# Kernel optimization log

Hardware: AMD Instinct MI355X
Metric: run time of the kernel (lower is better)

Reference implementation:

```python
import jax, jax.numpy as jnp
import numpy as np

BASE_BITS = 17            # tokens < 2**17; pack n-gram tuple into one int64
NGRAM_SIZES = (2, 3)      # sorted(ngram_to_size.keys())
TABLE_SIZE = 100000       # ngram_to_size[n]
ID_OFFSET = 4             # vocab ids start at 4 in the original
B, S, VOCAB = 256, 16384, 50000


def _encode_windows(x, n):
    """x: [B,S] int tokens -> [B,S] int64, each entry encodes the left-padded
    n-gram window (t[i-n+1],...,t[i]) exactly like the original tuple key."""
    b, s = x.shape
    padded = jnp.pad(x.astype(jnp.int64), ((0, 0), (n - 1, 0)))  # constant 0 pad, as in np.pad
    enc = jnp.zeros((b, s), dtype=jnp.int64)
    for i in range(n):  # tiny fixed loop over window size
        enc = (enc << BASE_BITS) | padded[:, i:i + s]
    return enc


def _lookup(enc, keys, vals):
    """dict.get(tuple(window), 0) as sorted-array hash-probe: searchsorted + verify."""
    flat = enc.reshape(-1)
    idx = jnp.clip(jnp.searchsorted(keys, flat), 0, keys.shape[0] - 1)
    hit = keys[idx] == flat
    return jnp.where(hit, vals[idx], 0).reshape(enc.shape)


def setup_inputs() -> dict:
    rng = np.random.default_rng(0)
    x = rng.integers(0, VOCAB, size=(B, S), dtype=np.int64)
    inp = {"x": jnp.asarray(x)}
    xj = jnp.asarray(x)
    for n in NGRAM_SIZES:
        # Build vocab tables from n-grams actually present so lookups hit,
        # mirroring update_from_batch() having seen similar data.
        enc = np.asarray(_encode_windows(xj, n)).reshape(-1)
        uniq = np.unique(enc)
        take = min(TABLE_SIZE, uniq.size)
        keys = np.sort(rng.choice(uniq, size=take, replace=False)).astype(np.int64)
        vals = (rng.permutation(take) + ID_OFFSET).astype(np.int64)  # ids 4..take+3
        inp[f"keys{n}"] = jnp.asarray(keys)
        inp[f"vals{n}"] = jnp.asarray(vals)
    return inp


def reference(x, keys2, vals2, keys3, vals3):
    tables = {2: (keys2, vals2), 3: (keys3, vals3)}
    # encode_token_ngrams + stack_ngrams -> [len(NGRAM_SIZES), B, S]
    outs = [_lookup(_encode_windows(x, n), *tables[n]) for n in NGRAM_SIZES]
    return jnp.stack(outs, axis=0)
```

## Files before the change

kernel.cpp:

```cpp
#include <hip/hip_runtime.h>

#define BASE_BITS 17
#define BUCKET_LOG 16
#define NBUCKETS (1u << BUCKET_LOG)
#define NSLOTS (NBUCKETS * 4u)
#define SLOT_MASK (NSLOTS - 1u)
#define BUCKET_MASK (NBUCKETS - 1u)
#define EMPTY 0xFFFFFFFFu

typedef int  iv4 __attribute__((ext_vector_type(4)));
typedef unsigned uv4 __attribute__((ext_vector_type(4)));

__device__ __forceinline__ unsigned bucket_of(unsigned k) {
    return (k * 2654435761u) >> (32 - BUCKET_LOG);
}

__device__ __forceinline__ int match4(uv4 q, unsigned e, unsigned b) {
    int slot = -1;
    slot = (q.w == e) ? (int)(b * 4u + 3u) : slot;
    slot = (q.z == e) ? (int)(b * 4u + 2u) : slot;
    slot = (q.y == e) ? (int)(b * 4u + 1u) : slot;
    slot = (q.x == e) ? (int)(b * 4u + 0u) : slot;
    if (slot >= 0) return slot;
    unsigned mx = max(max(q.x, q.y), max(q.z, q.w));
    return (mx == EMPTY) ? -2 : -1;
}

__global__ void clear_tables_kernel(uv4* __restrict__ dst, unsigned n4) {
    unsigned i = blockIdx.x * blockDim.x + threadIdx.x;
    unsigned stride = gridDim.x * blockDim.x;
    uv4 ones = { EMPTY, EMPTY, EMPTY, EMPTY };
    for (; i < n4; i += stride) __builtin_nontemporal_store(ones, &dst[i]);
}

__global__ void detect_dtype_kernel(const unsigned* __restrict__ xw,
                                    int* __restrict__ flags) {
    __shared__ int nz;
    if (threadIdx.x == 0) nz = 0;
    __syncthreads();
    if (xw[2 * threadIdx.x + 1] != 0u) atomicOr(&nz, 1);
    __syncthreads();
    if (threadIdx.x == 0) { flags[0] = nz ? 0 : ~0; flags[1] = 0; }
}

__global__ void build_hash_kernel(const int* __restrict__ keys2,
                                  const int* __restrict__ vals2, int n2,
                                  const int* __restrict__ keys3,
                                  const int* __restrict__ vals3, int n3,
                                  const unsigned* __restrict__ xw,
                                  unsigned* __restrict__ K2, int* __restrict__ V2,
                                  unsigned* __restrict__ K3, int* __restrict__ V3,
                                  int* __restrict__ flags) {
    int i = blockIdx.x * blockDim.x + threadIdx.x;
    if (i < 256 && xw[2 * i + 1] != 0u) atomicAnd(&flags[0], 0);

    const int* keys; const int* vals; unsigned* K; int* V; int idx;
    if (i < n2)           { keys = keys2; vals = vals2; K = K2; V = V2; idx = i; }
    else if (i < n2 + n3) { keys = keys3; vals = vals3; K = K3; V = V3; idx = i - n2; }
    else return;
    unsigned k = (unsigned)keys[idx];
    if (k == EMPTY) { atomicAnd(&flags[1], 0); return; }
    unsigned slot = bucket_of(k) * 4u;
    for (;;) {
        unsigned prev = atomicCAS(&K[slot], EMPTY, k);
        if (prev == EMPTY) { V[slot] = vals[idx]; break; }
        slot = (slot + 1u) & SLOT_MASK;
    }
}

template <typename K>
__device__ __forceinline__ int lower_bound(const K* __restrict__ keys, int n, K key) {
    int lo = 0, hi = n;
    while (lo < hi) {
        int mid = (lo + hi) >> 1;
        if (keys[mid] < key) lo = mid + 1; else hi = mid;
    }
    return lo;
}

template <typename K>
__device__ __forceinline__ K bprobe(const K* __restrict__ keys,
                                    const K* __restrict__ vals, int n, K key) {
    int idx = lower_bound(keys, n, key);
    if (idx >= n) idx = n - 1;
    return (keys[idx] == key) ? vals[idx] : (K)0;
}

__global__ __launch_bounds__(256) void ngram_hash_kernel(
    const void* __restrict__ xv,
    const unsigned* __restrict__ K2, const int* __restrict__ V2,
    const unsigned* __restrict__ K3, const int* __restrict__ V3,
    const void* __restrict__ k2v, const void* __restrict__ v2v,
    const void* __restrict__ k3v, const void* __restrict__ v3v,
    void* __restrict__ outv,
    int n2, int n3, int S, int total, const int* __restrict__ flags)
{
    int gid = blockIdx.x * blockDim.x + threadIdx.x;
    int base = gid * 4;
    if (base >= total) return;
    int f0 = flags[0], f1 = flags[1];

    if (f0 != 0) {
        const long long* x = (const long long*)xv;
        long long* out = (long long*)outv;
        for (int i = 0; i < 4 && base + i < total; ++i) {
            int g = base + i;
            int s = g & (S - 1);
            long long t2 = x[g];
            long long t1 = (s >= 1) ? x[g - 1] : 0ll;
            long long t0 = (s >= 2) ? x[g - 2] : 0ll;
            long long e2 = (t1 << BASE_BITS) | t2;
            long long e3 = (((t0 << BASE_BITS) | t1) << BASE_BITS) | t2;
            out[g]         = bprobe((const long long*)k2v, (const long long*)v2v, n2, e2);
            out[total + g] = bprobe((const long long*)k3v, (const long long*)v3v, n3, e3);
        }
        return;
    }
    if (f1 == 0) {
        const int* x = (const int*)xv;
        int* out = (int*)outv;
        for (int i = 0; i < 4 && base + i < total; ++i) {
            int g = base + i;
            int s = g & (S - 1);
            unsigned t2 = (unsigned)x[g];
            unsigned t1 = (s >= 1) ? (unsigned)x[g - 1] : 0u;
            unsigned t0 = (s >= 2) ? (unsigned)x[g - 2] : 0u;
            int e2 = (int)((t1 << BASE_BITS) | t2);
            int e3 = (int)((((t0 << BASE_BITS) | t1) << BASE_BITS) | t2);
            out[g]         = bprobe((const int*)k2v, (const int*)v2v, n2, e2);
            out[total + g] = bprobe((const int*)k3v, (const int*)v3v, n3, e3);
        }
        return;
    }

    const int* x = (const int*)xv;
    iv4 xq = __builtin_nontemporal_load(&((const iv4*)x)[gid]);
    int sb = base & (S - 1);
    unsigned t[6];
    t[0] = (sb != 0) ? (unsigned)x[base - 2] : 0u;
    t[1] = (sb != 0) ? (unsigned)x[base - 1] : 0u;
    t[2] = (unsigned)xq.x; t[3] = (unsigned)xq.y;
    t[4] = (unsigned)xq.z; t[5] = (unsigned)xq.w;

    unsigned e[8], b[8];
    #pragma unroll
    for (int i = 0; i < 4; ++i) {
        unsigned t0 = t[i], t1 = t[i + 1], t2 = t[i + 2];
        e[i]     = (t1 << BASE_BITS) | t2;
        e[i + 4] = (((t0 << BASE_BITS) | t1) << BASE_BITS) | t2;
    }
    #pragma unroll
    for (int i = 0; i < 8; ++i) b[i] = bucket_of(e[i]);

    const uv4* KB2 = (const uv4*)K2;
    const uv4* KB3 = (const uv4*)K3;

    const uv4* a0 = KB2 + b[0]; const uv4* a1 = KB2 + b[1];
    const uv4* a2 = KB2 + b[2]; const uv4* a3 = KB2 + b[3];
    const uv4* a4 = KB3 + b[4]; const uv4* a5 = KB3 + b[5];
    const uv4* a6 = KB3 + b[6]; const uv4* a7 = KB3 + b[7];
    uv4 q0, q1, q2, q3, q4, q5, q6, q7;
    asm volatile(
        "global_load_dwordx4 %0, %8, off\n\t"
        "global_load_dwordx4 %1, %9, off\n\t"
        "global_load_dwordx4 %2, %10, off\n\t"
        "global_load_dwordx4 %3, %11, off\n\t"
        "global_load_dwordx4 %4, %12, off\n\t"
        "global_load_dwordx4 %5, %13, off\n\t"
        "global_load_dwordx4 %6, %14, off\n\t"
        "global_load_dwordx4 %7, %15, off\n\t"
        "s_waitcnt vmcnt(0)"
        : "=&v"(q0), "=&v"(q1), "=&v"(q2), "=&v"(q3),
          "=&v"(q4), "=&v"(q5), "=&v"(q6), "=&v"(q7)
        : "v"(a0), "v"(a1), "v"(a2), "v"(a3),
          "v"(a4), "v"(a5), "v"(a6), "v"(a7)
        : "memory");

    int st[8];
    st[0] = match4(q0, e[0], b[0]);
    st[1] = match4(q1, e[1], b[1]);
    st[2] = match4(q2, e[2], b[2]);
    st[3] = match4(q3, e[3], b[3]);
    st[4] = match4(q4, e[4], b[4]);
    st[5] = match4(q5, e[5], b[5]);
    st[6] = match4(q6, e[6], b[6]);
    st[7] = match4(q7, e[7], b[7]);

    bool cont = false;
    #pragma unroll
    for (int i = 0; i < 8; ++i) cont |= (st[i] == -1);
    while (__any(cont)) {
        #pragma unroll
        for (int i = 0; i < 8; ++i) {
            if (st[i] == -1) {
                b[i] = (b[i] + 1u) & BUCKET_MASK;
                uv4 nq = (i < 4 ? KB2 : KB3)[b[i]];
                st[i] = match4(nq, e[i], b[i]);
            }
        }
        cont = false;
        #pragma unroll
        for (int i = 0; i < 8; ++i) cont |= (st[i] == -1);
    }

    int r[8];
    #pragma unroll
    for (int i = 0; i < 8; ++i)
        r[i] = (st[i] >= 0) ? (i < 4 ? V2 : V3)[st[i]] : 0;

    iv4 o2 = { r[0], r[1], r[2], r[3] };
    iv4 o3 = { r[4], r[5], r[6], r[7] };
    __builtin_nontemporal_store(o2, &((iv4*)outv)[gid]);
    __builtin_nontemporal_store(o3, &((iv4*)outv)[total / 4 + gid]);
}

extern "C" void kernel_launch(void* const* d_in, const int* in_sizes, int n_in,
                              void* d_out, int out_size, void* d_ws, size_t ws_size,
                              hipStream_t stream) {
    const void* x  = d_in[0];
    const void* k2 = d_in[1];
    const void* v2 = d_in[2];
    const void* k3 = d_in[3];
    const void* v3 = d_in[4];
    int n2 = in_sizes[1];
    int n3 = in_sizes[3];
    int total = in_sizes[0];
    int S = 16384;

    int* flags = (int*)d_ws;
    size_t key_bytes = (size_t)NSLOTS * 4;
    size_t need = 256 + 4 * key_bytes;

    int block = 256;
    int grid = (total / 4 + block - 1) / block;

    if (ws_size >= need) {
        unsigned* K2 = (unsigned*)((char*)d_ws + 256);
        unsigned* K3 = K2 + NSLOTS;
        int* V2 = (int*)(K3 + NSLOTS);
        int* V3 = V2 + NSLOTS;

        unsigned clear_n4 = (unsigned)((256 + 2 * key_bytes) / 16);
        clear_tables_kernel<<<2048, 256, 0, stream>>>((uv4*)d_ws, clear_n4);

        build_hash_kernel<<<(n2 + n3 + 255) / 256, 256, 0, stream>>>(
            (const int*)k2, (const int*)v2, n2,
            (const int*)k3, (const int*)v3, n3,
            (const unsigned*)x, K2, V2, K3, V3, flags);

        ngram_hash_kernel<<<grid, block, 0, stream>>>(
            x, K2, V2, K3, V3, k2, v2, k3, v3, d_out, n2, n3, S, total, flags);
    } else {
        detect_dtype_kernel<<<1, 256, 0, stream>>>((const unsigned*)x, flags);
        ngram_hash_kernel<<<grid, block, 0, stream>>>(
            x, nullptr, nullptr, nullptr, nullptr,
            k2, v2, k3, v3, d_out, n2, n3, S, total, flags);
    }
}
```

Baseline: 89.92 us.

## Pack key and value into 64-bit hash slots to drop dependent value load

Restructures the hash table so each slot stores key and value together as a 64-bit word. Buckets go from four 32-bit key slots to two packed pairs, with twice as many buckets. The probe's 16-byte load now returns the values directly, which removes the second dependent gather into a separate value array. In exchange each bucket holds only two entries, so probe chains may get longer, and the clear kernel switches from nontemporal to regular stores.

```diff
diff --git a/kernel.cpp b/kernel.cpp
--- a/kernel.cpp
+++ b/kernel.cpp
@@ -1,12 +1,13 @@
 #include <hip/hip_runtime.h>
 
 #define BASE_BITS 17
-#define BUCKET_LOG 16
+#define BUCKET_LOG 17
 #define NBUCKETS (1u << BUCKET_LOG)
-#define NSLOTS (NBUCKETS * 4u)
+#define NSLOTS (NBUCKETS * 2u)
 #define SLOT_MASK (NSLOTS - 1u)
 #define BUCKET_MASK (NBUCKETS - 1u)
 #define EMPTY 0xFFFFFFFFu
+#define EMPTY64 0xFFFFFFFFFFFFFFFFull
 
 typedef int  iv4 __attribute__((ext_vector_type(4)));
 typedef unsigned uv4 __attribute__((ext_vector_type(4)));
@@ -15,22 +16,19 @@
     return (k * 2654435761u) >> (32 - BUCKET_LOG);
 }
 
-__device__ __forceinline__ int match4(uv4 q, unsigned e, unsigned b) {
-    int slot = -1;
-    slot = (q.w == e) ? (int)(b * 4u + 3u) : slot;
-    slot = (q.z == e) ? (int)(b * 4u + 2u) : slot;
-    slot = (q.y == e) ? (int)(b * 4u + 1u) : slot;
-    slot = (q.x == e) ? (int)(b * 4u + 0u) : slot;
-    if (slot >= 0) return slot;
-    unsigned mx = max(max(q.x, q.y), max(q.z, q.w));
-    return (mx == EMPTY) ? -2 : -1;
+__device__ __forceinline__ int match2(uv4 q, unsigned e) {
+    if (q.x == e)     return (int)q.y;
+    if (q.x == EMPTY) return 0;
+    if (q.z == e)     return (int)q.w;
+    if (q.z == EMPTY) return 0;
+    return -1;
 }
 
 __global__ void clear_tables_kernel(uv4* __restrict__ dst, unsigned n4) {
     unsigned i = blockIdx.x * blockDim.x + threadIdx.x;
     unsigned stride = gridDim.x * blockDim.x;
     uv4 ones = { EMPTY, EMPTY, EMPTY, EMPTY };
-    for (; i < n4; i += stride) __builtin_nontemporal_store(ones, &dst[i]);
+    for (; i < n4; i += stride) dst[i] = ones;
 }
 
 __global__ void detect_dtype_kernel(const unsigned* __restrict__ xw,
@@ -48,24 +46,23 @@
                                   const int* __restrict__ keys3,
                                   const int* __restrict__ vals3, int n3,
                                   const unsigned* __restrict__ xw,
-                                  unsigned* __restrict__ K2, int* __restrict__ V2,
-                                  unsigned* __restrict__ K3, int* __restrict__ V3,
+                                  unsigned long long* __restrict__ T2,
+                                  unsigned long long* __restrict__ T3,
                                   int* __restrict__ flags) {
     int i = blockIdx.x * blockDim.x + threadIdx.x;
     if (i < 256 && xw[2 * i + 1] != 0u) atomicAnd(&flags[0], 0);
 
-    const int* keys; const int* vals; unsigned* K; int* V; int idx;
-    if (i < n2)           { keys = keys2; vals = vals2; K = K2; V = V2; idx = i; }
-    else if (i < n2 + n3) { keys = keys3; vals = vals3; K = K3; V = V3; idx = i - n2; }
+    const int* keys; const int* vals; unsigned long long* T; int idx;
+    if (i < n2)           { keys = keys2; vals = vals2; T = T2; idx = i; }
+    else if (i < n2 + n3) { keys = keys3; vals = vals3; T = T3; idx = i - n2; }
     else return;
     unsigned k = (unsigned)keys[idx];
     if (k == EMPTY) { atomicAnd(&flags[1], 0); return; }
-    unsigned slot = bucket_of(k) * 4u;
-    for (;;) {
-        unsigned prev = atomicCAS(&K[slot], EMPTY, k);
-        if (prev == EMPTY) { V[slot] = vals[idx]; break; }
+    unsigned long long packed =
+        ((unsigned long long)(unsigned)vals[idx] << 32) | (unsigned long long)k;
+    unsigned slot = bucket_of(k) * 2u;
+    while (atomicCAS(&T[slot], EMPTY64, packed) != EMPTY64)
         slot = (slot + 1u) & SLOT_MASK;
-    }
 }
 
 template <typename K>
@@ -88,8 +85,8 @@
 
 __global__ __launch_bounds__(256) void ngram_hash_kernel(
     const void* __restrict__ xv,
-    const unsigned* __restrict__ K2, const int* __restrict__ V2,
-    const unsigned* __restrict__ K3, const int* __restrict__ V3,
+    const unsigned long long* __restrict__ T2,
+    const unsigned long long* __restrict__ T3,
     const void* __restrict__ k2v, const void* __restrict__ v2v,
     const void* __restrict__ k3v, const void* __restrict__ v3v,
     void* __restrict__ outv,
@@ -152,8 +149,8 @@
     #pragma unroll
     for (int i = 0; i < 8; ++i) b[i] = bucket_of(e[i]);
 
-    const uv4* KB2 = (const uv4*)K2;
-    const uv4* KB3 = (const uv4*)K3;
+    const uv4* KB2 = (const uv4*)T2;
+    const uv4* KB3 = (const uv4*)T3;
 
     const uv4* a0 = KB2 + b[0]; const uv4* a1 = KB2 + b[1];
     const uv4* a2 = KB2 + b[2]; const uv4* a3 = KB2 + b[3];
@@ -176,37 +173,32 @@
           "v"(a4), "v"(a5), "v"(a6), "v"(a7)
         : "memory");
 
-    int st[8];
-    st[0] = match4(q0, e[0], b[0]);
-    st[1] = match4(q1, e[1], b[1]);
-    st[2] = match4(q2, e[2], b[2]);
-    st[3] = match4(q3, e[3], b[3]);
-    st[4] = match4(q4, e[4], b[4]);
-    st[5] = match4(q5, e[5], b[5]);
-    st[6] = match4(q6, e[6], b[6]);
-    st[7] = match4(q7, e[7], b[7]);
+    int r[8];
+    r[0] = match2(q0, e[0]);
+    r[1] = match2(q1, e[1]);
+    r[2] = match2(q2, e[2]);
+    r[3] = match2(q3, e[3]);
+    r[4] = match2(q4, e[4]);
+    r[5] = match2(q5, e[5]);
+    r[6] = match2(q6, e[6]);
+    r[7] = match2(q7, e[7]);
 
     bool cont = false;
     #pragma unroll
-    for (int i = 0; i < 8; ++i) cont |= (st[i] == -1);
+    for (int i = 0; i < 8; ++i) cont |= (r[i] < 0);
     while (__any(cont)) {
         #pragma unroll
         for (int i = 0; i < 8; ++i) {
-            if (st[i] == -1) {
+            if (r[i] < 0) {
                 b[i] = (b[i] + 1u) & BUCKET_MASK;
                 uv4 nq = (i < 4 ? KB2 : KB3)[b[i]];
-                st[i] = match4(nq, e[i], b[i]);
+                r[i] = match2(nq, e[i]);
             }
         }
         cont = false;
         #pragma unroll
-        for (int i = 0; i < 8; ++i) cont |= (st[i] == -1);
-    }
-
-    int r[8];
-    #pragma unroll
-    for (int i = 0; i < 8; ++i)
-        r[i] = (st[i] >= 0) ? (i < 4 ? V2 : V3)[st[i]] : 0;
+        for (int i = 0; i < 8; ++i) cont |= (r[i] < 0);
+    }
 
     iv4 o2 = { r[0], r[1], r[2], r[3] };
     iv4 o3 = { r[4], r[5], r[6], r[7] };
@@ -228,32 +220,30 @@
     int S = 16384;
 
     int* flags = (int*)d_ws;
-    size_t key_bytes = (size_t)NSLOTS * 4;
-    size_t need = 256 + 4 * key_bytes;
+    size_t table_bytes = (size_t)NSLOTS * 8;
+    size_t need = 256 + 2 * table_bytes;
 
     int block = 256;
     int grid = (total / 4 + block - 1) / block;
 
     if (ws_size >= need) {
-        unsigned* K2 = (unsigned*)((char*)d_ws + 256);
-        unsigned* K3 = K2 + NSLOTS;
-        int* V2 = (int*)(K3 + NSLOTS);
-        int* V3 = V2 + NSLOTS;
-
-        unsigned clear_n4 = (unsigned)((256 + 2 * key_bytes) / 16);
+        unsigned long long* T2 = (unsigned long long*)((char*)d_ws + 256);
+        unsigned long long* T3 = T2 + NSLOTS;
+
+        unsigned clear_n4 = (unsigned)((256 + 2 * table_bytes) / 16);
         clear_tables_kernel<<<2048, 256, 0, stream>>>((uv4*)d_ws, clear_n4);
 
         build_hash_kernel<<<(n2 + n3 + 255) / 256, 256, 0, stream>>>(
             (const int*)k2, (const int*)v2, n2,
             (const int*)k3, (const int*)v3, n3,
-            (const unsigned*)x, K2, V2, K3, V3, flags);
+            (const unsigned*)x, T2, T3, flags);
 
         ngram_hash_kernel<<<grid, block, 0, stream>>>(
-            x, K2, V2, K3, V3, k2, v2, k3, v3, d_out, n2, n3, S, total, flags);
+            x, T2, T3, k2, v2, k3, v3, d_out, n2, n3, S, total, flags);
     } else {
         detect_dtype_kernel<<<1, 256, 0, stream>>>((const unsigned*)x, flags);
         ngram_hash_kernel<<<grid, block, 0, stream>>>(
-            x, nullptr, nullptr, nullptr, nullptr,
+            x, nullptr, nullptr,
             k2, v2, k3, v3, d_out, n2, n3, S, total, flags);
     }
 }
```

Result: slower. 105.6 us (+17.4%).
